# Optimization experiments

Measured on AMD Instinct MI355X. Metric: run time of the kernel, lower is better.

## Reference

```python
import jax, jax.numpy as jnp
import numpy as np

HEAD = 8
C = 32
SCALE = 1.0 / (C ** 0.5)


def setup_inputs() -> dict:
    key = jax.random.key(0)
    ks = jax.random.split(key, 6)
    N, S, R, M, Z = 1, 128, 256, 256, 128
    return {
        "msa_repr": jax.random.normal(ks[0], (N, S, R, M), jnp.float32),
        "pair_repr": jax.random.normal(ks[1], (N, R, R, Z), jnp.float32),
        "gate_proj": jax.random.normal(ks[2], (M, M), jnp.float32) * 0.05,
        "qkv_proj": jax.random.normal(ks[3], (M, 3 * M), jnp.float32) * 0.05,
        "out_proj": jax.random.normal(ks[4], (M, M), jnp.float32) * 0.05,
        "bias_proj": jax.random.normal(ks[5], (Z, HEAD), jnp.float32) * 0.05,
    }


def reference(msa_repr, pair_repr, gate_proj, qkv_proj, out_proj, bias_proj):
    bs, s, r, cm = msa_repr.shape
    head, c, scale = HEAD, C, SCALE
    # pair bias: [N,R,R,Z] @ [Z,H] -> [N,H,R,R], broadcast over S
    bias = jnp.einsum('nijz,zh->nhij', pair_repr, bias_proj)[:, None]  # N,1,H,R,R
    gate = jax.nn.sigmoid(msa_repr @ gate_proj).reshape(bs, s, r, head, c)
    q, k, v = jnp.split(msa_repr @ qkv_proj, 3, axis=-1)
    q = q.reshape(bs, s, r, head, c)
    k = k.reshape(bs, s, r, head, c)
    v = v.reshape(bs, s, r, head, c)
    sim = jnp.einsum('nsqhc,nskhc->nshqk', q, k) * scale  # N,S,H,R,R
    sim = jax.nn.softmax(sim, axis=-1)
    # NOTE: bias is added AFTER softmax, faithful to the original torch code
    sim = sim + bias
    attend = jnp.einsum('nshqk,nskhc->nsqhc', sim, v) * gate
    out = attend.reshape(bs, s, r, cm) @ out_proj
    return out
```

## Files before the change

kernel.cpp:

```cpp
#include <hip/hip_runtime.h>
#include <hip/hip_bf16.h>
#include <stdint.h>

#define SCALE 0.17677669529663687f

typedef short bf8 __attribute__((ext_vector_type(8)));
typedef float f32x4 __attribute__((ext_vector_type(4)));

__device__ __forceinline__ short f2bf(float f) {
  unsigned u = __builtin_bit_cast(unsigned, f);
  u = (u + 0x7FFFu + ((u >> 16) & 1u)) >> 16;
  return (short)u;
}
__device__ __forceinline__ float bf2f(short s) {
  return __builtin_bit_cast(float, ((unsigned)(unsigned short)s) << 16);
}
__device__ __forceinline__ void gl_lds16(const void* g, void* l) {
  __builtin_amdgcn_global_load_lds(
      (const __attribute__((address_space(1))) unsigned int*)g,
      (__attribute__((address_space(3))) unsigned int*)l, 16, 0, 0);
}

__global__ __launch_bounds__(256) void convert_msa(
    const float* __restrict__ in, short* __restrict__ out, int n4) {
  int i = blockIdx.x * 256 + threadIdx.x;
  const int stride = gridDim.x * 256;
  for (; i < n4; i += stride) {
    float4 v = ((const float4*)in)[i];
    short4 o;
    o.x = f2bf(v.x); o.y = f2bf(v.y); o.z = f2bf(v.z); o.w = f2bf(v.w);
    ((short4*)out)[i] = o;
  }
}

__global__ __launch_bounds__(256) void prep_w(
    const float* __restrict__ gw, const float* __restrict__ qw,
    const float* __restrict__ ow, short* __restrict__ wcat,
    short* __restrict__ owt) {
  int i = blockIdx.x * 256 + threadIdx.x;
  if (i < 262144) {
    int n = i >> 8, k = i & 255;
    wcat[i] = f2bf(n < 256 ? gw[k * 256 + n] : qw[k * 768 + (n - 256)]);
  } else if (i < 327680) {
    int j = i - 262144;
    int n = j >> 8, k = j & 255;
    owt[j] = f2bf(ow[k * 256 + n]);
  }
}

__global__ __launch_bounds__(256) void bias_kernel(
    const float* __restrict__ pair, const float* __restrict__ bias_w,
    short* __restrict__ bias) {
  __shared__ float Bp[1024];
  const int t = threadIdx.x;
  for (int i = t; i < 1024; i += 256) Bp[i] = bias_w[i];
  __syncthreads();

  const int ij = blockIdx.x * 256 + t;
  const float* pr = pair + (size_t)ij * 128;

  float acc[8] = {};
  for (int z4 = 0; z4 < 128; z4 += 4) {
    float4 pv = *(const float4*)&pr[z4];
    const float pe[4] = {pv.x, pv.y, pv.z, pv.w};
#pragma unroll
    for (int u = 0; u < 4; ++u)
#pragma unroll
      for (int h = 0; h < 8; ++h)
        acc[h] = fmaf(pe[u], Bp[(z4 + u) * 8 + h], acc[h]);
  }
#pragma unroll
  for (int h = 0; h < 8; ++h)
    bias[(size_t)h * 65536 + ij] = f2bf(acc[h]);
}

template <int MODE>
__global__ __launch_bounds__(256) void gemm_bf16(
    const short* __restrict__ A, const short* __restrict__ Bt,
    void* __restrict__ C0, void* __restrict__ C1, int M, int N, int K) {
  __shared__ short As[128 * 32];
  __shared__ short Bs[128 * 32];
  const int tid = threadIdx.x;
  const int lane = tid & 63, w = tid >> 6;
  const int l15 = lane & 15, l4 = lane >> 4;
  const int m0 = blockIdx.y * 128, n0 = blockIdx.x * 128;
  const int wm = (w >> 1) * 64, wn = (w & 1) * 64;

  f32x4 acc[4][4];
#pragma unroll
  for (int i = 0; i < 4; ++i)
#pragma unroll
    for (int j = 0; j < 4; ++j) acc[i][j] = (f32x4)(0.0f);

  const int srow = w * 32 + (lane >> 2);
  const int scol = (lane & 3) * 8;

  for (int k0 = 0; k0 < K; k0 += 32) {
    __syncthreads();
    gl_lds16(A + (size_t)(m0 + srow) * K + k0 + scol, &As[(w * 32) * 32]);
    gl_lds16(A + (size_t)(m0 + srow + 16) * K + k0 + scol, &As[(w * 32 + 16) * 32]);
    gl_lds16(Bt + (size_t)(n0 + srow) * K + k0 + scol, &Bs[(w * 32) * 32]);
    gl_lds16(Bt + (size_t)(n0 + srow + 16) * K + k0 + scol, &Bs[(w * 32 + 16) * 32]);
    __syncthreads();
#pragma unroll
    for (int nf = 0; nf < 4; ++nf) {
      bf8 bfr = *(const bf8*)(&Bs[(wn + nf * 16 + l15) * 32 + l4 * 8]);
#pragma unroll
      for (int mf = 0; mf < 4; ++mf) {
        bf8 afr = *(const bf8*)(&As[(wm + mf * 16 + l15) * 32 + l4 * 8]);
        acc[mf][nf] =
            __builtin_amdgcn_mfma_f32_16x16x32_bf16(afr, bfr, acc[mf][nf], 0, 0, 0);
      }
    }
  }

#pragma unroll
  for (int mf = 0; mf < 4; ++mf)
#pragma unroll
    for (int nf = 0; nf < 4; ++nf)
#pragma unroll
      for (int r = 0; r < 4; ++r) {
        const int m = m0 + wm + mf * 16 + l4 * 4 + r;
        const int n = n0 + wn + nf * 16 + l15;
        float v = acc[mf][nf][r];
        if (MODE == 0) {
          if (n < 256)
            ((short*)C0)[(size_t)m * 256 + n] = f2bf(1.0f / (1.0f + __expf(-v)));
          else
            ((short*)C1)[(size_t)m * 768 + (n - 256)] = f2bf(v);
        } else {
          ((float*)C0)[(size_t)m * N + n] = v;
        }
      }
}

__global__ __launch_bounds__(256) void attn_mfma(
    const short* __restrict__ qkv,
    const short* __restrict__ bias,
    const short* __restrict__ gate,
    short* __restrict__ attendg) {
  const int s = blockIdx.x >> 3;
  const int h = blockIdx.x & 7;
  const int tid = threadIdx.x;
  const int lane = tid & 63, w = tid >> 6;
  const int l15 = lane & 15, l4 = lane >> 4;

  __shared__ short Vt[32][264];
  __shared__ short Plds[4][64][72];

  {
    const short* vrow = qkv + (size_t)(s * 256 + tid) * 768 + 512 + h * 32;
    short tmp[32];
    *(int4*)(tmp +  0) = *(const int4*)(vrow +  0);
    *(int4*)(tmp +  8) = *(const int4*)(vrow +  8);
    *(int4*)(tmp + 16) = *(const int4*)(vrow + 16);
    *(int4*)(tmp + 24) = *(const int4*)(vrow + 24);
#pragma unroll
    for (int c = 0; c < 32; ++c) Vt[c][tid] = tmp[c];
  }

  bf8 qf[4];
  const int q0 = w * 64;
#pragma unroll
  for (int mf = 0; mf < 4; ++mf)
    qf[mf] = *(const bf8*)(qkv + (size_t)(s * 256 + q0 + mf * 16 + l15) * 768 +
                           h * 32 + l4 * 8);

  __syncthreads();

  f32x4 o1[4][2], o2[4][2];
  float lsum[16];
#pragma unroll
  for (int mf = 0; mf < 4; ++mf)
#pragma unroll
    for (int nf = 0; nf < 2; ++nf) {
      o1[mf][nf] = (f32x4)(0.0f);
      o2[mf][nf] = (f32x4)(0.0f);
    }
#pragma unroll
  for (int i = 0; i < 16; ++i) lsum[i] = 0.0f;

  for (int kb = 0; kb < 4; ++kb) {
    f32x4 sa[4][4];
#pragma unroll
    for (int nf = 0; nf < 4; ++nf) {
      bf8 kf = *(const bf8*)(qkv +
                             (size_t)(s * 256 + kb * 64 + nf * 16 + l15) * 768 +
                             256 + h * 32 + l4 * 8);
#pragma unroll
      for (int mf = 0; mf < 4; ++mf)
        sa[mf][nf] =
            __builtin_amdgcn_mfma_f32_16x16x32_bf16(qf[mf], kf, (f32x4)(0.0f), 0, 0, 0);
    }

    __syncthreads();
#pragma unroll
    for (int mf = 0; mf < 4; ++mf)
#pragma unroll
      for (int nf = 0; nf < 4; ++nf)
#pragma unroll
        for (int r = 0; r < 4; ++r) {
          float e = __expf(sa[mf][nf][r] * SCALE);
          lsum[mf * 4 + r] += e;
          Plds[w][mf * 16 + l4 * 4 + r][nf * 16 + l15] = f2bf(e);
        }
    __syncthreads();

#pragma unroll
    for (int ks = 0; ks < 2; ++ks) {
      bf8 vf[2];
#pragma unroll
      for (int nf = 0; nf < 2; ++nf)
        vf[nf] = *(const bf8*)(&Vt[nf * 16 + l15][kb * 64 + ks * 32 + l4 * 8]);
#pragma unroll
      for (int mf = 0; mf < 4; ++mf) {
        bf8 pf = *(const bf8*)(&Plds[w][mf * 16 + l15][ks * 32 + l4 * 8]);
        bf8 bfr = *(const bf8*)(bias + ((size_t)h * 256 + q0 + mf * 16 + l15) * 256 +
                                kb * 64 + ks * 32 + l4 * 8);
#pragma unroll
        for (int nf = 0; nf < 2; ++nf) {
          o1[mf][nf] = __builtin_amdgcn_mfma_f32_16x16x32_bf16(pf, vf[nf], o1[mf][nf], 0, 0, 0);
          o2[mf][nf] = __builtin_amdgcn_mfma_f32_16x16x32_bf16(bfr, vf[nf], o2[mf][nf], 0, 0, 0);
        }
      }
    }
  }

#pragma unroll
  for (int i = 0; i < 16; ++i) {
    float v = lsum[i];
    v += __shfl_xor(v, 1);
    v += __shfl_xor(v, 2);
    v += __shfl_xor(v, 4);
    v += __shfl_xor(v, 8);
    lsum[i] = 1.0f / v;
  }

#pragma unroll
  for (int mf = 0; mf < 4; ++mf)
#pragma unroll
    for (int nf = 0; nf < 2; ++nf)
#pragma unroll
      for (int r = 0; r < 4; ++r) {
        const int q = q0 + mf * 16 + l4 * 4 + r;
        const int c = nf * 16 + l15;
        const size_t off = (size_t)(s * 256 + q) * 256 + h * 32 + c;
        float val = o1[mf][nf][r] * lsum[mf * 4 + r] + o2[mf][nf][r];
        attendg[off] = f2bf(val * bf2f(gate[off]));
      }
}

extern "C" void kernel_launch(void* const* d_in, const int* in_sizes, int n_in,
                              void* d_out, int out_size, void* d_ws,
                              size_t ws_size, hipStream_t stream) {
  const float* msa    = (const float*)d_in[0];
  const float* pair   = (const float*)d_in[1];
  const float* gate_w = (const float*)d_in[2];
  const float* qkv_w  = (const float*)d_in[3];
  const float* out_w  = (const float*)d_in[4];
  const float* bias_w = (const float*)d_in[5];
  float* out = (float*)d_out;

  char* ws = (char*)d_ws;
  short* qkv_bf  = (short*)(ws);
  short* msa_bf  = (short*)(ws + 50331648);
  short* gate_bf = (short*)(ws + 67108864);
  short* attendg = (short*)(ws + 83886080);
  short* bias_bf = (short*)(ws + 100663296);
  short* wcat_t  = (short*)(ws + 101711872);
  short* owt     = (short*)(ws + 102236160);

  const int M = 32768;

  convert_msa<<<2048, 256, 0, stream>>>(msa, msa_bf, M * 256 / 4);
  prep_w<<<1280, 256, 0, stream>>>(gate_w, qkv_w, out_w, wcat_t, owt);
  bias_kernel<<<256, 256, 0, stream>>>(pair, bias_w, bias_bf);

  gemm_bf16<0><<<dim3(8, M / 128), 256, 0, stream>>>(
      msa_bf, wcat_t, gate_bf, qkv_bf, M, 1024, 256);

  attn_mfma<<<1024, 256, 0, stream>>>(qkv_bf, bias_bf, gate_bf, attendg);

  gemm_bf16<1><<<dim3(2, M / 128), 256, 0, stream>>>(
      attendg, owt, out, nullptr, M, 256, 256);
}
```

Baseline: 238.2 us.

## Double-buffer GEMM LDS, fold softmax scale into Q, drop attention barriers

The GEMM now double-buffers its LDS tiles with explicit vmcnt waits, so global-to-LDS loads overlap the MFMA work. The Q projection epilogue pre-multiplies by scale·log2(e), letting attention use exp2 with no per-element multiply. The attention kernel removes the block-wide barriers around the per-wave P buffer, changes P padding, and adds s_setprio hints around MFMA phases. The main risks are alignment of 16-byte LDS reads with the new 68-element row pitch and subtler intra-wave ordering.

```diff
diff --git a/kernel.cpp b/kernel.cpp
--- a/kernel.cpp
+++ b/kernel.cpp
@@ -2,7 +2,7 @@
 #include <hip/hip_bf16.h>
 #include <stdint.h>
 
-#define SCALE 0.17677669529663687f
+#define QSCALE 0.2550348552724541f
 
 typedef short bf8 __attribute__((ext_vector_type(8)));
 typedef float f32x4 __attribute__((ext_vector_type(4)));
@@ -78,8 +78,8 @@
 __global__ __launch_bounds__(256) void gemm_bf16(
     const short* __restrict__ A, const short* __restrict__ Bt,
     void* __restrict__ C0, void* __restrict__ C1, int M, int N, int K) {
-  __shared__ short As[128 * 32];
-  __shared__ short Bs[128 * 32];
+  __shared__ short As[2][128 * 32];
+  __shared__ short Bs[2][128 * 32];
   const int tid = threadIdx.x;
   const int lane = tid & 63, w = tid >> 6;
   const int l15 = lane & 15, l4 = lane >> 4;
@@ -95,23 +95,39 @@
   const int srow = w * 32 + (lane >> 2);
   const int scol = (lane & 3) * 8;
 
-  for (int k0 = 0; k0 < K; k0 += 32) {
-    __syncthreads();
-    gl_lds16(A + (size_t)(m0 + srow) * K + k0 + scol, &As[(w * 32) * 32]);
-    gl_lds16(A + (size_t)(m0 + srow + 16) * K + k0 + scol, &As[(w * 32 + 16) * 32]);
-    gl_lds16(Bt + (size_t)(n0 + srow) * K + k0 + scol, &Bs[(w * 32) * 32]);
-    gl_lds16(Bt + (size_t)(n0 + srow + 16) * K + k0 + scol, &Bs[(w * 32 + 16) * 32]);
-    __syncthreads();
+  auto stage = [&](int buf, int k0) {
+    gl_lds16(A + (size_t)(m0 + srow) * K + k0 + scol, &As[buf][(w * 32) * 32]);
+    gl_lds16(A + (size_t)(m0 + srow + 16) * K + k0 + scol,
+             &As[buf][(w * 32 + 16) * 32]);
+    gl_lds16(Bt + (size_t)(n0 + srow) * K + k0 + scol, &Bs[buf][(w * 32) * 32]);
+    gl_lds16(Bt + (size_t)(n0 + srow + 16) * K + k0 + scol,
+             &Bs[buf][(w * 32 + 16) * 32]);
+  };
+
+  const int NT = K >> 5;
+  stage(0, 0);
+  for (int t = 0; t < NT; ++t) {
+    const int cur = t & 1;
+    if (t + 1 < NT) {
+      stage(cur ^ 1, (t + 1) << 5);
+      asm volatile("s_waitcnt vmcnt(4)" ::: "memory");
+    } else {
+      asm volatile("s_waitcnt vmcnt(0)" ::: "memory");
+    }
+    __builtin_amdgcn_s_barrier();
+    __builtin_amdgcn_sched_barrier(0);
 #pragma unroll
     for (int nf = 0; nf < 4; ++nf) {
-      bf8 bfr = *(const bf8*)(&Bs[(wn + nf * 16 + l15) * 32 + l4 * 8]);
+      bf8 bfr = *(const bf8*)(&Bs[cur][(wn + nf * 16 + l15) * 32 + l4 * 8]);
 #pragma unroll
       for (int mf = 0; mf < 4; ++mf) {
-        bf8 afr = *(const bf8*)(&As[(wm + mf * 16 + l15) * 32 + l4 * 8]);
+        bf8 afr = *(const bf8*)(&As[cur][(wm + mf * 16 + l15) * 32 + l4 * 8]);
         acc[mf][nf] =
             __builtin_amdgcn_mfma_f32_16x16x32_bf16(afr, bfr, acc[mf][nf], 0, 0, 0);
       }
     }
+    __builtin_amdgcn_sched_barrier(0);
+    __builtin_amdgcn_s_barrier();
   }
 
 #pragma unroll
@@ -124,10 +140,12 @@
         const int n = n0 + wn + nf * 16 + l15;
         float v = acc[mf][nf][r];
         if (MODE == 0) {
-          if (n < 256)
+          if (n < 256) {
             ((short*)C0)[(size_t)m * 256 + n] = f2bf(1.0f / (1.0f + __expf(-v)));
-          else
+          } else {
+            if (n < 512) v *= QSCALE;
             ((short*)C1)[(size_t)m * 768 + (n - 256)] = f2bf(v);
+          }
         } else {
           ((float*)C0)[(size_t)m * N + n] = v;
         }
@@ -146,7 +164,7 @@
   const int l15 = lane & 15, l4 = lane >> 4;
 
   __shared__ short Vt[32][264];
-  __shared__ short Plds[4][64][72];
+  __shared__ short Plds[4][64][68];
 
   {
     const short* vrow = qkv + (size_t)(s * 256 + tid) * 768 + 512 + h * 32;
@@ -182,6 +200,7 @@
 
   for (int kb = 0; kb < 4; ++kb) {
     f32x4 sa[4][4];
+    __builtin_amdgcn_s_setprio(1);
 #pragma unroll
     for (int nf = 0; nf < 4; ++nf) {
       bf8 kf = *(const bf8*)(qkv +
@@ -192,20 +211,20 @@
         sa[mf][nf] =
             __builtin_amdgcn_mfma_f32_16x16x32_bf16(qf[mf], kf, (f32x4)(0.0f), 0, 0, 0);
     }
-
-    __syncthreads();
+    __builtin_amdgcn_s_setprio(0);
+
 #pragma unroll
     for (int mf = 0; mf < 4; ++mf)
 #pragma unroll
       for (int nf = 0; nf < 4; ++nf)
 #pragma unroll
         for (int r = 0; r < 4; ++r) {
-          float e = __expf(sa[mf][nf][r] * SCALE);
+          float e = exp2f(sa[mf][nf][r]);
           lsum[mf * 4 + r] += e;
           Plds[w][mf * 16 + l4 * 4 + r][nf * 16 + l15] = f2bf(e);
         }
-    __syncthreads();
-
+
+    __builtin_amdgcn_s_setprio(1);
 #pragma unroll
     for (int ks = 0; ks < 2; ++ks) {
       bf8 vf[2];
@@ -224,6 +243,7 @@
         }
       }
     }
+    __builtin_amdgcn_s_setprio(0);
   }
 
 #pragma unroll
```

Measured after the change: 236.9 us. About the same (-0.6%).
